# Performance work log

Measured on AMD Instinct MI355X. Metric: run time of the kernel, lower is better.

## Reference

```python
import jax, jax.numpy as jnp
import numpy as np

H = 256          # hidden_size
L = 2            # num_layers
K = 4            # khops
R = 128          # relation_num
N_NODES = 20000
N_EDGES = 160000
N_LG_EDGES = 640000


def setup_inputs() -> dict:
    key = jax.random.key(0)
    ks = iter(jax.random.split(key, 40))
    def nrm(shape, s=1.0):
        return jax.random.normal(next(ks), shape, dtype=jnp.float32) * s
    w = 1.0 / float(np.sqrt(H))
    return {
        "x": nrm((N_NODES, H)),
        "edge_feat": jax.random.randint(next(ks), (N_EDGES,), 0, R),
        "edge_index_g": jax.random.randint(next(ks), (2, N_EDGES), 0, N_NODES),
        "edge_index_lg": jax.random.randint(next(ks), (2, N_LG_EDGES), 0, N_EDGES),
        "rel_embed": nrm((R, H)),
        # per-layer, per-core (0=node update, 1=edge update) parameter stacks
        "w_self": nrm((L, 2, H, H), w), "b_self": jnp.zeros((L, 2, H), jnp.float32),
        "w_khop": nrm((L, 2, K, H, H), w), "b_khop": jnp.zeros((L, 2, K, H), jnp.float32),
        "w_fuse": nrm((L, 2, H, H), w), "b_fuse": jnp.zeros((L, 2, H), jnp.float32),
        "w_ff1": nrm((L, 2, H, 4 * H), w), "b_ff1": jnp.zeros((L, 2, 4 * H), jnp.float32),
        "w_ff2": nrm((L, 2, 4 * H, H), 1.0 / float(np.sqrt(4 * H))), "b_ff2": jnp.zeros((L, 2, H), jnp.float32),
        "ln1_g": jnp.ones((L, 2, H), jnp.float32), "ln1_b": jnp.zeros((L, 2, H), jnp.float32),
        "ln2_g": jnp.ones((L, 2, H), jnp.float32), "ln2_b": jnp.zeros((L, 2, H), jnp.float32),
    }


def _layernorm(x, g, b, eps=1e-5):
    m = jnp.mean(x, axis=-1, keepdims=True)
    v = jnp.var(x, axis=-1, keepdims=True)
    return (x - m) * jax.lax.rsqrt(v + eps) * g + b


def _core(p, src, dst, x, fused):
    """LGNNCore.forward (eval mode, dropout never applied in core)."""
    (ws, bs, wk, bk, wf, bf, w1, b1, w2, b2, g1, c1, g2, c2) = p
    n = x.shape[0]
    prev = x @ ws + bs
    # k-hop copy_src + sum aggregation, each hop gets its own linear
    z = x
    kh = jnp.zeros_like(prev)
    for i in range(wk.shape[0]):
        z = jax.ops.segment_sum(z[src], dst, num_segments=n)
        kh = kh + z @ wk[i] + bk[i]
    edge = fused @ wf + bf
    out = jax.nn.gelu(prev + kh + edge, approximate=False)
    out = _layernorm(x + out, g1, c1)
    ffn = jax.nn.gelu(out @ w1 + b1, approximate=False) @ w2 + b2
    return _layernorm(out + ffn, g2, c2)


def reference(x, edge_feat, edge_index_g, edge_index_lg, rel_embed,
              w_self, b_self, w_khop, b_khop, w_fuse, b_fuse,
              w_ff1, b_ff1, w_ff2, b_ff2, ln1_g, ln1_b, ln2_g, ln2_b):
    lg_x = rel_embed[edge_feat]                       # [n_edges, H]
    src_g, dst_g = edge_index_g[0], edge_index_g[1]
    src_l, dst_l = edge_index_lg[0], edge_index_lg[1]
    n_nodes = x.shape[0]
    for l in range(w_self.shape[0]):
        def pick(c):
            return (w_self[l, c], b_self[l, c], w_khop[l, c], b_khop[l, c],
                    w_fuse[l, c], b_fuse[l, c], w_ff1[l, c], b_ff1[l, c],
                    w_ff2[l, c], b_ff2[l, c], ln1_g[l, c], ln1_b[l, c],
                    ln2_g[l, c], ln2_b[l, c])
        # pmpd @ lg_x : scatter each edge feature to both of its endpoints
        fused_nodes = (jax.ops.segment_sum(lg_x, src_g, num_segments=n_nodes)
                       + jax.ops.segment_sum(lg_x, dst_g, num_segments=n_nodes))
        # pmpd^T @ x : gather both endpoint node features per edge
        fused_edges = x[src_g] + x[dst_g]
        new_x = _core(pick(0), src_g, dst_g, x, fused_nodes)
        new_lg_x = _core(pick(1), src_l, dst_l, lg_x, fused_edges)
        x, lg_x = new_x, new_lg_x
    return x, lg_x
```

## Files before the change

### kernel.cpp

```cpp
#include <hip/hip_runtime.h>

typedef __bf16 bf16;
typedef __attribute__((ext_vector_type(8))) __bf16 bf16x8;
typedef __attribute__((ext_vector_type(4))) __bf16 bf16x4;
typedef __attribute__((ext_vector_type(4))) float f32x4;

#define HD 256
#define GEMM_GELU 2

__device__ __forceinline__ float gelu_f(float x) {
  float x2 = x * x;
  float u = 1.5957691216057308f * x * fmaf(0.044715f, x2, 1.0f);
  float e = __expf(-u);
  return x / (1.0f + e);
}

__device__ __forceinline__ void gload_lds16(const void* g, void* l) {
  __builtin_amdgcn_global_load_lds(
      (const __attribute__((address_space(1))) unsigned int*)g,
      (__attribute__((address_space(3))) unsigned int*)l, 16, 0, 0);
}

__global__ __launch_bounds__(256) void gemm_k(
    const bf16* __restrict__ A, const bf16* __restrict__ Wt,
    const float* __restrict__ bias, bf16* __restrict__ C,
    int M, int Kd, int lda, int ldc, int flags)
{
  __shared__ __align__(16) bf16 sA[2][128 * 32];
  __shared__ __align__(16) bf16 sB[2][128 * 32];
  const int t = threadIdx.x;
  const int lane = t & 63, w = t >> 6;
  const int n0 = blockIdx.x * 128, m0 = blockIdx.y * 128;
  const int wr = w >> 1, wc = w & 1;
  const int lm = lane & 15, quad = lane >> 4;

  const int srow = t >> 2;
  const int cg = (t & 3) ^ ((t >> 3) & 3);
  const bool full = (m0 + 128 <= M);

  const char* a0 = (const char*)(A + (size_t)(m0 + srow) * lda) + cg * 16;
  const char* a1 = (const char*)(A + (size_t)(m0 + srow + 64) * lda) + cg * 16;
  const char* b0 = (const char*)(Wt + (size_t)(n0 + srow) * Kd) + cg * 16;
  const char* b1 = (const char*)(Wt + (size_t)(n0 + srow) * Kd) + (size_t)64 * Kd * 2 + cg * 16;

  const int soff = (quad ^ ((lm >> 1) & 3)) * 8;

  f32x4 acc[4][4];
#pragma unroll
  for (int i = 0; i < 4; i++)
#pragma unroll
    for (int j = 0; j < 4; j++)
#pragma unroll
      for (int r = 0; r < 4; r++) acc[i][j][r] = 0.f;

  const int nk = Kd >> 5;

  auto stage = [&](int buf, int kb) {
    size_t ko = (size_t)kb * 2;
    bf16* SA = sA[buf];
    bf16* SB = sB[buf];
    if (full) {
      gload_lds16(a0 + ko, SA + w * 512);
      gload_lds16(a1 + ko, SA + 2048 + w * 512);
    } else {
#pragma unroll
      for (int c = 0; c < 2; c++) {
        int row = srow + c * 64;
        int gr = m0 + row;
        bf16x8 va;
#pragma unroll
        for (int q = 0; q < 8; q++) va[q] = (bf16)0.f;
        if (gr < M) va = *(const bf16x8*)((const char*)(A + (size_t)gr * lda) + ko + cg * 16);
        *(bf16x8*)(SA + row * 32 + (t & 3) * 8) = va;
      }
    }
    gload_lds16(b0 + ko, SB + w * 512);
    gload_lds16(b1 + ko, SB + 2048 + w * 512);
  };

  auto compute = [&](int buf) {
    const bf16* SA = sA[buf];
    const bf16* SB = sB[buf];
    bf16x8 af[4], bv[4];
#pragma unroll
    for (int i = 0; i < 4; i++) af[i] = *(const bf16x8*)(SA + (wr * 64 + i * 16 + lm) * 32 + soff);
#pragma unroll
    for (int j = 0; j < 4; j++) bv[j] = *(const bf16x8*)(SB + (wc * 64 + j * 16 + lm) * 32 + soff);
#pragma unroll
    for (int i = 0; i < 4; i++)
#pragma unroll
      for (int j = 0; j < 4; j++)
        acc[i][j] = __builtin_amdgcn_mfma_f32_16x16x32_bf16(bv[j], af[i], acc[i][j], 0, 0, 0);
  };

  stage(0, 0);
  __syncthreads();
  int cur = 0;
  for (int kt = 0; kt < nk - 1; ++kt) {
    stage(cur ^ 1, (kt + 1) << 5);
    compute(cur);
    __syncthreads();
    cur ^= 1;
  }
  compute(cur);

  float4 bia[4];
#pragma unroll
  for (int j = 0; j < 4; j++)
    bia[j] = *(const float4*)(bias + n0 + wc * 64 + j * 16 + quad * 4);
#pragma unroll
  for (int i = 0; i < 4; i++) {
    int gr = m0 + wr * 64 + i * 16 + lm;
    if (gr < M) {
      bf16* crow = C + (size_t)gr * ldc;
#pragma unroll
      for (int j = 0; j < 4; j++) {
        int gc = n0 + wc * 64 + j * 16 + quad * 4;
        float v0 = acc[i][j][0] + bia[j].x;
        float v1 = acc[i][j][1] + bia[j].y;
        float v2 = acc[i][j][2] + bia[j].z;
        float v3 = acc[i][j][3] + bia[j].w;
        if (flags & GEMM_GELU) {
          v0 = gelu_f(v0); v1 = gelu_f(v1); v2 = gelu_f(v2); v3 = gelu_f(v3);
        }
        bf16x4 o = {(bf16)v0, (bf16)v1, (bf16)v2, (bf16)v3};
        *(bf16x4*)(crow + gc) = o;
      }
    }
  }
}

__global__ __launch_bounds__(256) void segsum_k(
    const int* __restrict__ offs, const int* __restrict__ cols,
    const bf16* __restrict__ in, int ldin, bf16* __restrict__ out, int ldout, int nseg)
{
  int wid = threadIdx.x >> 6, lane = threadIdx.x & 63;
  int seg = blockIdx.x * 4 + wid;
  if (seg >= nseg) return;
  int b = offs[seg], e = offs[seg + 1];
  float a0 = 0.f, a1 = 0.f, a2 = 0.f, a3 = 0.f;
  for (int i = b; i < e; i++) {
    int c = cols[i];
    bf16x4 v = *(const bf16x4*)(in + (size_t)c * ldin + lane * 4);
    a0 += (float)v.x; a1 += (float)v.y; a2 += (float)v.z; a3 += (float)v.w;
  }
  bf16x4 o = {(bf16)a0, (bf16)a1, (bf16)a2, (bf16)a3};
  *(bf16x4*)(out + (size_t)seg * ldout + lane * 4) = o;
}

__global__ __launch_bounds__(256) void ln_k(
    const bf16* __restrict__ X, int ldx, const bf16* __restrict__ A,
    const float* __restrict__ gam, const float* __restrict__ bet,
    bf16* __restrict__ outb, float* __restrict__ outf, int M, int apply_gelu)
{
  int wid = threadIdx.x >> 6, lane = threadIdx.x & 63;
  int row = blockIdx.x * 4 + wid;
  if (row >= M) return;
  size_t xbase = (size_t)row * ldx + lane * 4;
  size_t abase = (size_t)row * HD + lane * 4;
  bf16x4 xv = *(const bf16x4*)(X + xbase);
  bf16x4 av = *(const bf16x4*)(A + abase);
  float s0, s1, s2, s3;
  if (apply_gelu) {
    s0 = (float)xv.x + gelu_f((float)av.x);
    s1 = (float)xv.y + gelu_f((float)av.y);
    s2 = (float)xv.z + gelu_f((float)av.z);
    s3 = (float)xv.w + gelu_f((float)av.w);
  } else {
    s0 = (float)xv.x + (float)av.x;
    s1 = (float)xv.y + (float)av.y;
    s2 = (float)xv.z + (float)av.z;
    s3 = (float)xv.w + (float)av.w;
  }
  float sum = s0 + s1 + s2 + s3;
#pragma unroll
  for (int o = 32; o; o >>= 1) sum += __shfl_xor(sum, o, 64);
  float mean = sum * (1.0f / 256.0f);
  float d0 = s0 - mean, d1 = s1 - mean, d2 = s2 - mean, d3 = s3 - mean;
  float vs = d0 * d0 + d1 * d1 + d2 * d2 + d3 * d3;
#pragma unroll
  for (int o = 32; o; o >>= 1) vs += __shfl_xor(vs, o, 64);
  float rstd = rsqrtf(vs * (1.0f / 256.0f) + 1e-5f);
  float4 g = *(const float4*)(gam + lane * 4);
  float4 bb = *(const float4*)(bet + lane * 4);
  float y0 = d0 * rstd * g.x + bb.x;
  float y1 = d1 * rstd * g.y + bb.y;
  float y2 = d2 * rstd * g.z + bb.z;
  float y3 = d3 * rstd * g.w + bb.w;
  if (outb) {
    bf16x4 o = {(bf16)y0, (bf16)y1, (bf16)y2, (bf16)y3};
    *(bf16x4*)(outb + xbase) = o;
  }
  if (outf) {
    float4 o = {y0, y1, y2, y3};
    *(float4*)(outf + abase) = o;
  }
}

__global__ __launch_bounds__(256) void gather_rel_k(
    const int* __restrict__ feat, const float* __restrict__ rel,
    bf16* __restrict__ out, int ldout, int NE)
{
  int wid = threadIdx.x >> 6, lane = threadIdx.x & 63;
  int e = blockIdx.x * 4 + wid;
  if (e >= NE) return;
  int f = feat[e];
  float4 v = *(const float4*)(rel + (size_t)f * HD + lane * 4);
  bf16x4 o = {(bf16)v.x, (bf16)v.y, (bf16)v.z, (bf16)v.w};
  *(bf16x4*)(out + (size_t)e * ldout + lane * 4) = o;
}

__global__ __launch_bounds__(256) void gather2_k(
    const int* __restrict__ src, const int* __restrict__ dst,
    const bf16* __restrict__ x, int ldx, bf16* __restrict__ out, int ldout, int NE)
{
  int wid = threadIdx.x >> 6, lane = threadIdx.x & 63;
  int e = blockIdx.x * 4 + wid;
  if (e >= NE) return;
  int s = src[e], d = dst[e];
  bf16x4 a = *(const bf16x4*)(x + (size_t)s * ldx + lane * 4);
  bf16x4 b = *(const bf16x4*)(x + (size_t)d * ldx + lane * 4);
  bf16x4 o = {(bf16)((float)a.x + (float)b.x), (bf16)((float)a.y + (float)b.y),
              (bf16)((float)a.z + (float)b.z), (bf16)((float)a.w + (float)b.w)};
  *(bf16x4*)(out + (size_t)e * ldout + lane * 4) = o;
}

__global__ __launch_bounds__(256) void f2b_k(const float* __restrict__ in,
                                             bf16* __restrict__ out, int ldout, int M) {
  int wid = threadIdx.x >> 6, lane = threadIdx.x & 63;
  int row = blockIdx.x * 4 + wid;
  if (row >= M) return;
  float4 v = *(const float4*)(in + (size_t)row * HD + lane * 4);
  bf16x4 o = {(bf16)v.x, (bf16)v.y, (bf16)v.z, (bf16)v.w};
  *(bf16x4*)(out + (size_t)row * ldout + lane * 4) = o;
}

__global__ __launch_bounds__(256) void wtrans_k(const float* __restrict__ in, bf16* __restrict__ out,
                                                int Kd, int Nd) {
  size_t moff = (size_t)blockIdx.y * Kd * Nd;
  int id = blockIdx.x * 256 + threadIdx.x;
  if (id >= Kd * Nd) return;
  int n = id / Kd, k = id - n * Kd;
  out[moff + id] = (bf16)in[moff + (size_t)k * Nd + n];
}

__global__ __launch_bounds__(256) void wcat_k(const float* __restrict__ ws, const float* __restrict__ wk,
                                              const float* __restrict__ wf, bf16* __restrict__ out,
                                              int KH, int CW) {
  int mi = blockIdx.y;
  int id = blockIdx.x * 256 + threadIdx.x;
  if (id >= HD * CW) return;
  int n = id / CW, k = id - n * CW;
  int s = k >> 8, kk = k & 255;
  float v;
  if (s == 0)       v = ws[((size_t)mi * HD + kk) * HD + n];
  else if (s <= KH) v = wk[(((size_t)mi * KH + (s - 1)) * HD + kk) * HD + n];
  else              v = wf[((size_t)mi * HD + kk) * HD + n];
  out[(size_t)mi * HD * CW + id] = (bf16)v;
}

__global__ __launch_bounds__(256) void bcat_k(const float* __restrict__ bs, const float* __restrict__ bk,
                                              const float* __restrict__ bf, float* __restrict__ out, int KH) {
  int mi = blockIdx.x, n = threadIdx.x;
  float v = bs[(size_t)mi * HD + n] + bf[(size_t)mi * HD + n];
  for (int i = 0; i < KH; i++) v += bk[((size_t)mi * KH + i) * HD + n];
  out[(size_t)mi * HD + n] = v;
}

__global__ __launch_bounds__(256) void count_k(const int* __restrict__ keys, int n, int* __restrict__ cnt) {
  int i = blockIdx.x * 256 + threadIdx.x;
  if (i < n) atomicAdd(&cnt[keys[i]], 1);
}
__global__ __launch_bounds__(256) void scan1_k(const int* __restrict__ in, int* __restrict__ out,
                                               int* __restrict__ bsum, int n) {
  __shared__ int sh[256];
  int t = threadIdx.x;
  int i0 = blockIdx.x * 1024 + t * 4;
  int v0 = (i0 < n) ? in[i0] : 0;
  int v1 = (i0 + 1 < n) ? in[i0 + 1] : 0;
  int v2 = (i0 + 2 < n) ? in[i0 + 2] : 0;
  int v3 = (i0 + 3 < n) ? in[i0 + 3] : 0;
  int tsum = v0 + v1 + v2 + v3;
  sh[t] = tsum;
  __syncthreads();
  for (int o = 1; o < 256; o <<= 1) {
    int x = (t >= o) ? sh[t - o] : 0;
    __syncthreads();
    sh[t] += x;
    __syncthreads();
  }
  int e0 = sh[t] - tsum;
  if (t == 255) bsum[blockIdx.x] = sh[255];
  if (i0 < n) out[i0] = e0;
  e0 += v0;
  if (i0 + 1 < n) out[i0 + 1] = e0;
  e0 += v1;
  if (i0 + 2 < n) out[i0 + 2] = e0;
  e0 += v2;
  if (i0 + 3 < n) out[i0 + 3] = e0;
}
__global__ void scan2_k(int* bsum, int nb, int* total) {
  if (threadIdx.x == 0 && blockIdx.x == 0) {
    int acc = 0;
    for (int i = 0; i < nb; i++) { int v = bsum[i]; bsum[i] = acc; acc += v; }
    *total = acc;
  }
}
__global__ __launch_bounds__(256) void scan3_k(int* out, const int* bsum, int n) {
  int i = blockIdx.x * 256 + threadIdx.x;
  if (i < n) out[i] += bsum[i >> 10];
}
__global__ __launch_bounds__(256) void fill_k(const int* __restrict__ keys, const int* __restrict__ vals,
                                              int n, int modE, int* __restrict__ cursor, int* __restrict__ cols) {
  int i = blockIdx.x * 256 + threadIdx.x;
  if (i >= n) return;
  int pos = atomicAdd(&cursor[keys[i]], 1);
  cols[pos] = vals ? vals[i] : (i < modE ? i : i - modE);
}

extern "C" void kernel_launch(void* const* d_in, const int* in_sizes, int n_in,
                              void* d_out, int out_size, void* d_ws, size_t ws_size,
                              hipStream_t stream)
{
  const float* x_in      = (const float*)d_in[0];
  const int*   edge_feat = (const int*)d_in[1];
  const int*   eig       = (const int*)d_in[2];
  const int*   eil       = (const int*)d_in[3];
  const float* rel       = (const float*)d_in[4];
  const float* w_self = (const float*)d_in[5];
  const float* b_self = (const float*)d_in[6];
  const float* w_khop = (const float*)d_in[7];
  const float* b_khop = (const float*)d_in[8];
  const float* w_fuse = (const float*)d_in[9];
  const float* b_fuse = (const float*)d_in[10];
  const float* w_ff1  = (const float*)d_in[11];
  const float* b_ff1  = (const float*)d_in[12];
  const float* w_ff2  = (const float*)d_in[13];
  const float* b_ff2  = (const float*)d_in[14];
  const float* ln1_g  = (const float*)d_in[15];
  const float* ln1_b  = (const float*)d_in[16];
  const float* ln2_g  = (const float*)d_in[17];
  const float* ln2_b  = (const float*)d_in[18];

  const int NN = in_sizes[0] / HD;
  const int NE = in_sizes[1];
  const int NL = in_sizes[3] / 2;
  const int L  = in_sizes[5] / (2 * HD * HD);
  const int KH = in_sizes[7] / (L * 2 * HD * HD);
  const int CW = (KH + 2) * HD;

  char* p = (char*)d_ws;
  auto alloc = [&](size_t bytes) -> void* {
    void* r = (void*)p;
    p += (bytes + 255) & ~(size_t)255;
    return r;
  };

  bf16* n_cat  = (bf16*)alloc((size_t)NN * CW * 2);
  bf16* lg_cat = (bf16*)alloc((size_t)NE * CW * 2);
  bf16* acc_n  = (bf16*)alloc((size_t)NN * HD * 2);
  bf16* acc_e  = (bf16*)alloc((size_t)NE * HD * 2);

  bf16*  wcat_t = (bf16*)alloc((size_t)L * 2 * HD * CW * 2);
  float* bcat   = (float*)alloc((size_t)L * 2 * HD * 4);
  bf16*  wff1_t = (bf16*)alloc((size_t)L * 2 * HD * 4 * HD * 2);
  bf16*  wff2_t = (bf16*)alloc((size_t)L * 2 * HD * 4 * HD * 2);

  int* inc_offs = (int*)alloc((size_t)(NN + 1) * 4);
  int* inc_cur  = (int*)alloc((size_t)NN * 4);
  int* inc_cols = (int*)alloc((size_t)2 * NE * 4);
  int* ng_offs  = (int*)alloc((size_t)(NN + 1) * 4);
  int* ng_cur   = (int*)alloc((size_t)NN * 4);
  int* ng_cols  = (int*)alloc((size_t)NE * 4);
  int* lg_offs  = (int*)alloc((size_t)(NE + 1) * 4);
  int* lg_cur   = (int*)alloc((size_t)NE * 4);
  int* lg_cols  = (int*)alloc((size_t)NL * 4);
  int* bsum     = (int*)alloc(3 * 256 * 4);

  wcat_k<<<dim3((HD * CW + 255) / 256, L * 2), 256, 0, stream>>>(w_self, w_khop, w_fuse, wcat_t, KH, CW);
  bcat_k<<<L * 2, 256, 0, stream>>>(b_self, b_khop, b_fuse, bcat, KH);
  wtrans_k<<<dim3((HD * 4 * HD + 255) / 256, L * 2), 256, 0, stream>>>(w_ff1, wff1_t, HD, 4 * HD);
  wtrans_k<<<dim3((HD * 4 * HD + 255) / 256, L * 2), 256, 0, stream>>>(w_ff2, wff2_t, 4 * HD, HD);

  f2b_k<<<(NN + 3) / 4, 256, 0, stream>>>(x_in, n_cat, CW, NN);
  gather_rel_k<<<(NE + 3) / 4, 256, 0, stream>>>(edge_feat, rel, lg_cat, CW, NE);

  auto build_csr = [&](const int* keys, int nkeys, const int* vals, int modE,
                       int nseg, int* offs, int* cur, int* cols, int* bs) {
    int nb = (nseg + 1023) / 1024;
    hipMemsetAsync(offs, 0, (size_t)(nseg + 1) * 4, stream);
    count_k<<<(nkeys + 255) / 256, 256, 0, stream>>>(keys, nkeys, offs);
    scan1_k<<<nb, 256, 0, stream>>>(offs, offs, bs, nseg);
    scan2_k<<<1, 1, 0, stream>>>(bs, nb, offs + nseg);
    scan3_k<<<(nseg + 255) / 256, 256, 0, stream>>>(offs, bs, nseg);
    hipMemcpyAsync(cur, offs, (size_t)nseg * 4, hipMemcpyDeviceToDevice, stream);
    fill_k<<<(nkeys + 255) / 256, 256, 0, stream>>>(keys, vals, nkeys, modE, cur, cols);
  };
  build_csr(eig, 2 * NE, nullptr, NE, NN, inc_offs, inc_cur, inc_cols, bsum);
  build_csr(eig + NE, NE, eig, 0, NN, ng_offs, ng_cur, ng_cols, bsum + 256);
  build_csr(eil + NL, NL, eil, 0, NE, lg_offs, lg_cur, lg_cols, bsum + 512);

  float* out_x  = (float*)d_out;
  float* out_lg = (float*)d_out + (size_t)NN * HD;

  auto run_core = [&](bf16* cat, bf16* accb, const int* coffs, const int* ccols,
                      int M, int l, int c, float* outf) {
    size_t mi = (size_t)(l * 2 + c);
    int mb = (M + 127) / 128;
    for (int i = 1; i <= KH; i++)
      segsum_k<<<(M + 3) / 4, 256, 0, stream>>>(coffs, ccols, cat + (size_t)(i - 1) * HD, CW,
                                                cat + (size_t)i * HD, CW, M);
    gemm_k<<<dim3(2, mb), 256, 0, stream>>>(cat, wcat_t + mi * HD * CW, bcat + mi * HD,
                                            accb, M, CW, CW, HD, 0);
    ln_k<<<(M + 3) / 4, 256, 0, stream>>>(cat, CW, accb, ln1_g + mi * HD, ln1_b + mi * HD,
                                          cat, (float*)nullptr, M, 1);
    bf16* hid = cat + HD;
    int FC = (M > 40000) ? 40000 : M;
    for (int c0 = 0; c0 < M; c0 += FC) {
      int mc = (M - c0 < FC) ? (M - c0) : FC;
      int mbc = (mc + 127) / 128;
      gemm_k<<<dim3(8, mbc), 256, 0, stream>>>(cat + (size_t)c0 * CW, wff1_t + mi * HD * 4 * HD,
                                               b_ff1 + mi * 4 * HD, hid, mc, HD, CW, CW, GEMM_GELU);
      gemm_k<<<dim3(2, mbc), 256, 0, stream>>>(hid, wff2_t + mi * 4 * HD * HD, b_ff2 + mi * HD,
                                               accb + (size_t)c0 * HD, mc, 4 * HD, CW, HD, 0);
    }
    ln_k<<<(M + 3) / 4, 256, 0, stream>>>(cat, CW, accb, ln2_g + mi * HD, ln2_b + mi * HD,
                                          cat, outf, M, 0);
  };

  for (int l = 0; l < L; l++) {
    segsum_k<<<(NN + 3) / 4, 256, 0, stream>>>(inc_offs, inc_cols, lg_cat, CW,
                                               n_cat + (size_t)(KH + 1) * HD, CW, NN);
    gather2_k<<<(NE + 3) / 4, 256, 0, stream>>>(eig, eig + NE, n_cat, CW,
                                                lg_cat + (size_t)(KH + 1) * HD, CW, NE);
    run_core(n_cat, acc_n, ng_offs, ng_cols, NN, l, 0, (l == L - 1) ? out_x : nullptr);
    run_core(lg_cat, acc_e, lg_offs, lg_cols, NE, l, 1, (l == L - 1) ? out_lg : nullptr);
  }
}
```

Baseline: 3.268 ms.

## Triple-buffer GEMM LDS tiles with explicit vmcnt waits for deeper prefetch

New measurement: 3.316 ms. No clear change (+1.5%).

```diff
diff --git a/kernel.cpp b/kernel.cpp
--- a/kernel.cpp
+++ b/kernel.cpp
@@ -26,8 +26,8 @@
     const float* __restrict__ bias, bf16* __restrict__ C,
     int M, int Kd, int lda, int ldc, int flags)
 {
-  __shared__ __align__(16) bf16 sA[2][128 * 32];
-  __shared__ __align__(16) bf16 sB[2][128 * 32];
+  __shared__ __align__(16) bf16 sA[3][128 * 32];
+  __shared__ __align__(16) bf16 sB[3][128 * 32];
   const int t = threadIdx.x;
   const int lane = t & 63, w = t >> 6;
   const int n0 = blockIdx.x * 128, m0 = blockIdx.y * 128;
@@ -55,14 +55,50 @@
 
   const int nk = Kd >> 5;
 
-  auto stage = [&](int buf, int kb) {
-    size_t ko = (size_t)kb * 2;
-    bf16* SA = sA[buf];
-    bf16* SB = sB[buf];
-    if (full) {
-      gload_lds16(a0 + ko, SA + w * 512);
-      gload_lds16(a1 + ko, SA + 2048 + w * 512);
-    } else {
+  auto stage = [&](bf16* SA, bf16* SB, int kt) {
+    size_t ko = (size_t)kt * 64;
+    gload_lds16(a0 + ko, SA + w * 512);
+    gload_lds16(a1 + ko, SA + 2048 + w * 512);
+    gload_lds16(b0 + ko, SB + w * 512);
+    gload_lds16(b1 + ko, SB + 2048 + w * 512);
+  };
+
+  auto compute = [&](const bf16* SA, const bf16* SB) {
+    bf16x8 af[4], bv[4];
+#pragma unroll
+    for (int i = 0; i < 4; i++) af[i] = *(const bf16x8*)(SA + (wr * 64 + i * 16 + lm) * 32 + soff);
+#pragma unroll
+    for (int j = 0; j < 4; j++) bv[j] = *(const bf16x8*)(SB + (wc * 64 + j * 16 + lm) * 32 + soff);
+#pragma unroll
+    for (int i = 0; i < 4; i++)
+#pragma unroll
+      for (int j = 0; j < 4; j++)
+        acc[i][j] = __builtin_amdgcn_mfma_f32_16x16x32_bf16(bv[j], af[i], acc[i][j], 0, 0, 0);
+  };
+
+  if (full) {
+    stage(sA[0], sB[0], 0);
+    if (nk > 1) stage(sA[1], sB[1], 1);
+    for (int kt = 0; kt < nk; ++kt) {
+      int cb = kt % 3;
+      int nxt = kt + 2;
+      if (nxt < nk) {
+        stage(sA[nxt % 3], sB[nxt % 3], nxt);
+        asm volatile("s_waitcnt vmcnt(8)" ::: "memory");
+      } else if (nxt == nk) {
+        asm volatile("s_waitcnt vmcnt(4)" ::: "memory");
+      } else {
+        asm volatile("s_waitcnt vmcnt(0)" ::: "memory");
+      }
+      __builtin_amdgcn_s_barrier();
+      asm volatile("" ::: "memory");
+      compute(sA[cb], sB[cb]);
+      __builtin_amdgcn_s_barrier();
+      asm volatile("" ::: "memory");
+    }
+  } else {
+    for (int kt = 0; kt < nk; ++kt) {
+      size_t ko = (size_t)kt * 64;
 #pragma unroll
       for (int c = 0; c < 2; c++) {
         int row = srow + c * 64;
@@ -71,38 +107,15 @@
 #pragma unroll
         for (int q = 0; q < 8; q++) va[q] = (bf16)0.f;
         if (gr < M) va = *(const bf16x8*)((const char*)(A + (size_t)gr * lda) + ko + cg * 16);
-        *(bf16x8*)(SA + row * 32 + (t & 3) * 8) = va;
+        *(bf16x8*)(sA[0] + row * 32 + (t & 3) * 8) = va;
       }
+      gload_lds16(b0 + ko, sB[0] + w * 512);
+      gload_lds16(b1 + ko, sB[0] + 2048 + w * 512);
+      __syncthreads();
+      compute(sA[0], sB[0]);
+      __syncthreads();
     }
-    gload_lds16(b0 + ko, SB + w * 512);
-    gload_lds16(b1 + ko, SB + 2048 + w * 512);
-  };
-
-  auto compute = [&](int buf) {
-    const bf16* SA = sA[buf];
-    const bf16* SB = sB[buf];
-    bf16x8 af[4], bv[4];
-#pragma unroll
-    for (int i = 0; i < 4; i++) af[i] = *(const bf16x8*)(SA + (wr * 64 + i * 16 + lm) * 32 + soff);
-#pragma unroll
-    for (int j = 0; j < 4; j++) bv[j] = *(const bf16x8*)(SB + (wc * 64 + j * 16 + lm) * 32 + soff);
-#pragma unroll
-    for (int i = 0; i < 4; i++)
-#pragma unroll
-      for (int j = 0; j < 4; j++)
-        acc[i][j] = __builtin_amdgcn_mfma_f32_16x16x32_bf16(bv[j], af[i], acc[i][j], 0, 0, 0);
-  };
-
-  stage(0, 0);
-  __syncthreads();
-  int cur = 0;
-  for (int kt = 0; kt < nk - 1; ++kt) {
-    stage(cur ^ 1, (kt + 1) << 5);
-    compute(cur);
-    __syncthreads();
-    cur ^= 1;
-  }
-  compute(cur);
+  }
 
   float4 bia[4];
 #pragma unroll
```
